# Performance work log

Measured on AMD Instinct MI355X. Metric: run time of the kernel, lower is better.

## Reference

```python
import jax, jax.numpy as jnp
import numpy as np
from jax import lax

FILTERS = 8      # Conv1D filters per column
K = 5            # kernel_size
ACTION_DIM = 2
COLS = [16, 128, 1024]  # columns entering each of the 3 blocks (grow x FILTERS)


def setup_inputs() -> dict:
    key = jax.random.key(0)
    ks = jax.random.split(key, 8)
    B, L, C = 64, 128, 16
    state = jax.random.normal(ks[0], (B, L, C), jnp.float32)
    inp = {"state": state}
    # One grouped-conv kernel per block: WIO layout [K, in_per_group=1, cols*FILTERS].
    # Channel c*FILTERS+f of the output is column c's filter f (matches Keras concat order).
    for i, c in enumerate(COLS):
        inp[f"k{i+1}"] = jax.random.normal(ks[1 + i], (K, 1, c * FILTERS), jnp.float32) * 0.1
        inp[f"b{i+1}"] = jnp.zeros((c * FILTERS,), jnp.float32)
    L_final = L - len(COLS) * (K - 1)          # 116
    feat = L_final * COLS[-1] * FILTERS        # 950272
    inp["W"] = jax.random.normal(ks[4], (feat, ACTION_DIM), jnp.float32) * 1e-3
    inp["bd"] = jnp.zeros((ACTION_DIM,), jnp.float32)
    return inp


def _block(x, kern, bias):
    # x: [B, cols, L]  ->  [B, cols*FILTERS, L-K+1]
    cols = x.shape[1]
    xin = jnp.transpose(x, (0, 2, 1))  # [B, L, cols] (NWC)
    y = lax.conv_general_dilated(
        xin, kern, window_strides=(1,), padding='VALID',
        dimension_numbers=('NWC', 'WIO', 'NWC'), feature_group_count=cols)
    y = jax.nn.relu(y + bias)          # [B, L', cols*FILTERS]
    return jnp.transpose(y, (0, 2, 1))


def reference(state, k1, b1, k2, b2, k3, b3, W, bd):
    # Actor.call: transpose [B,L,C] -> [B,C,L], run blocks, transpose back, flatten, dense+tanh
    x = jnp.transpose(state, (0, 2, 1))  # [B, cols=16, L=128]
    for kern, bias in ((k1, b1), (k2, b2), (k3, b3)):
        x = _block(x, kern, bias)
    x = jnp.transpose(x, (0, 2, 1)).reshape(state.shape[0], -1)  # [B, L'*channels]
    return jnp.tanh(x @ W + bd)  # [B, ACTION_DIM]
```

## Files before the change

kernel.cpp:

```cpp
#include <hip/hip_runtime.h>
#include <math.h>

#define NB    64
#define L0    128
#define C0    16
#define KW    5
#define NF    8
#define L1    124
#define L2    120
#define L3    116
#define CH1   128
#define CH2   1024
#define CH3   8192
#define NCHUNK 8
#define NS     4
#define SLICE  29
#define TROWS  (SLICE + 4)
#define Y1R    (SLICE + 8)
#define STR    (SLICE + 12)

__global__ __launch_bounds__(128, 4) void actor_fused_kernel(
    const float* __restrict__ state,
    const float* __restrict__ k1,
    const float* __restrict__ b1,
    const float* __restrict__ k2,
    const float* __restrict__ b2,
    const float* __restrict__ k3,
    const float* __restrict__ b3,
    const float* __restrict__ W,
    float* __restrict__ partials)
{
    const int chunk = blockIdx.x;
    const int b     = blockIdx.y;
    const int slice = blockIdx.z;
    const int t0    = slice * SLICE;
    const int tid   = threadIdx.x;
    const int c3    = chunk * 128 + tid;

    __shared__ float s_state[STR][2];
    __shared__ float s_y1[Y1R][16];
    __shared__ float tile[TROWS][128];

    for (int idx = tid; idx < STR * 2; idx += 128) {
        int r = idx >> 1, c = idx & 1;
        s_state[r][c] = state[(size_t)b * L0 * C0 + (t0 + r) * C0 + chunk * 2 + c];
    }
    __syncthreads();

    for (int idx = tid; idx < Y1R * 16; idx += 128) {
        int r = idx >> 4, jloc = idx & 15;
        int j = chunk * 16 + jloc;
        int cloc = jloc >> 3;
        float acc = b1[j];
#pragma unroll
        for (int k = 0; k < KW; ++k)
            acc = fmaf(s_state[r + k][cloc], k1[k * CH1 + j], acc);
        s_y1[r][jloc] = fmaxf(acc, 0.f);
    }
    __syncthreads();

    {
        int m = chunk * 128 + tid;
        int jloc = tid >> 3;
        float kk[KW], bb = b2[m];
#pragma unroll
        for (int k = 0; k < KW; ++k) kk[k] = k2[k * CH2 + m];
        for (int r = 0; r < TROWS; ++r) {
            float acc = bb;
#pragma unroll
            for (int k = 0; k < KW; ++k)
                acc = fmaf(s_y1[r + k][jloc], kk[k], acc);
            tile[r][tid] = fmaxf(acc, 0.f);
        }
    }

    float kw[KW][NF], bv[NF];
#pragma unroll
    for (int k = 0; k < KW; ++k)
#pragma unroll
        for (int f = 0; f < NF; ++f)
            kw[k][f] = k3[k * CH3 + c3 * NF + f];
#pragma unroll
    for (int f = 0; f < NF; ++f)
        bv[f] = b3[c3 * NF + f];

    float a0x = 0.f, a0y = 0.f, a1x = 0.f, a1y = 0.f;
    float a2x = 0.f, a2y = 0.f, a3x = 0.f, a3y = 0.f;

    const float4* __restrict__ W4 = (const float4*)W;

    float w0 = tile[0][tid];
    float w1 = tile[1][tid];
    float w2 = tile[2][tid];
    float w3 = tile[3][tid];

    for (int t = 0; t < SLICE; ++t) {
        float w4 = tile[t + 4][tid];

        float v[NF];
#pragma unroll
        for (int f = 0; f < NF; ++f) {
            float a = bv[f];
            a = fmaf(w0, kw[0][f], a);
            a = fmaf(w1, kw[1][f], a);
            a = fmaf(w2, kw[2][f], a);
            a = fmaf(w3, kw[3][f], a);
            a = fmaf(w4, kw[4][f], a);
            v[f] = fmaxf(a, 0.f);
        }

        size_t base4 = (size_t)(t0 + t) * 4096 + (size_t)c3 * 4;
        float4 q0 = W4[base4 + 0];
        float4 q1 = W4[base4 + 1];
        float4 q2 = W4[base4 + 2];
        float4 q3 = W4[base4 + 3];

        a0x = fmaf(v[0], q0.x, a0x); a0y = fmaf(v[0], q0.y, a0y);
        a0x = fmaf(v[1], q0.z, a0x); a0y = fmaf(v[1], q0.w, a0y);
        a1x = fmaf(v[2], q1.x, a1x); a1y = fmaf(v[2], q1.y, a1y);
        a1x = fmaf(v[3], q1.z, a1x); a1y = fmaf(v[3], q1.w, a1y);
        a2x = fmaf(v[4], q2.x, a2x); a2y = fmaf(v[4], q2.y, a2y);
        a2x = fmaf(v[5], q2.z, a2x); a2y = fmaf(v[5], q2.w, a2y);
        a3x = fmaf(v[6], q3.x, a3x); a3y = fmaf(v[6], q3.y, a3y);
        a3x = fmaf(v[7], q3.z, a3x); a3y = fmaf(v[7], q3.w, a3y);

        w0 = w1; w1 = w2; w2 = w3; w3 = w4;
    }

    float acc0 = (a0x + a1x) + (a2x + a3x);
    float acc1 = (a0y + a1y) + (a2y + a3y);

#pragma unroll
    for (int d = 32; d >= 1; d >>= 1) {
        acc0 += __shfl_down(acc0, d, 64);
        acc1 += __shfl_down(acc1, d, 64);
    }
    __shared__ float red[2][2];
    int wave = tid >> 6, lane = tid & 63;
    if (lane == 0) { red[wave][0] = acc0; red[wave][1] = acc1; }
    __syncthreads();
    if (tid == 0) {
        size_t o = (((size_t)b * NCHUNK + chunk) * NS + slice) * 2;
        partials[o + 0] = red[0][0] + red[1][0];
        partials[o + 1] = red[0][1] + red[1][1];
    }
}

__global__ __launch_bounds__(128) void finish_kernel(
    const float* __restrict__ partials,
    const float* __restrict__ bd,
    float* __restrict__ out)
{
    int i = threadIdx.x;
    int b = i >> 1, a = i & 1;
    float s = bd[a];
#pragma unroll
    for (int p = 0; p < NCHUNK * NS; ++p)
        s += partials[((size_t)b * NCHUNK * NS + p) * 2 + a];
    out[b * 2 + a] = tanhf(s);
}

extern "C" void kernel_launch(void* const* d_in, const int* in_sizes, int n_in,
                              void* d_out, int out_size, void* d_ws, size_t ws_size,
                              hipStream_t stream) {
    const float* state = (const float*)d_in[0];
    const float* k1    = (const float*)d_in[1];
    const float* b1    = (const float*)d_in[2];
    const float* k2    = (const float*)d_in[3];
    const float* b2    = (const float*)d_in[4];
    const float* k3    = (const float*)d_in[5];
    const float* b3    = (const float*)d_in[6];
    const float* W     = (const float*)d_in[7];
    const float* bd    = (const float*)d_in[8];
    float* out = (float*)d_out;

    float* partials = (float*)d_ws;

    dim3 grid(NCHUNK, NB, NS);
    actor_fused_kernel<<<grid, 128, 0, stream>>>(
        state, k1, b1, k2, b2, k3, b3, W, partials);

    finish_kernel<<<1, 128, 0, stream>>>(partials, bd, out);
}
```

Before: 105.3 us.

## Split each layer-3 column's filters across two threads with 256-thread blocks

Doubles the block size to 256 threads. Each pair of threads now handles one layer-3 column, each taking half of the 8 filters and half of the W float4 loads. The layer-2 tile computation is split between the two 128-thread halves, and a barrier is added because threads now read tile columns written by other threads. This halves per-thread registers and serial work to raise occupancy and memory-level parallelism. The cost is redundant tile reads and an extra barrier.

After: 98.38 us. -6.5%, faster.

```diff
diff --git a/kernel.cpp b/kernel.cpp
--- a/kernel.cpp
+++ b/kernel.cpp
@@ -18,8 +18,9 @@
 #define TROWS  (SLICE + 4)
 #define Y1R    (SLICE + 8)
 #define STR    (SLICE + 12)
+#define NFH    4
 
-__global__ __launch_bounds__(128, 4) void actor_fused_kernel(
+__global__ __launch_bounds__(256, 8) void actor_fused_kernel(
     const float* __restrict__ state,
     const float* __restrict__ k1,
     const float* __restrict__ b1,
@@ -35,19 +36,21 @@
     const int slice = blockIdx.z;
     const int t0    = slice * SLICE;
     const int tid   = threadIdx.x;
-    const int c3    = chunk * 128 + tid;
+    const int c3loc = tid >> 1;
+    const int fh    = tid & 1;
+    const int c3    = chunk * 128 + c3loc;
 
     __shared__ float s_state[STR][2];
     __shared__ float s_y1[Y1R][16];
     __shared__ float tile[TROWS][128];
 
-    for (int idx = tid; idx < STR * 2; idx += 128) {
-        int r = idx >> 1, c = idx & 1;
+    if (tid < STR * 2) {
+        int r = tid >> 1, c = tid & 1;
         s_state[r][c] = state[(size_t)b * L0 * C0 + (t0 + r) * C0 + chunk * 2 + c];
     }
     __syncthreads();
 
-    for (int idx = tid; idx < Y1R * 16; idx += 128) {
+    for (int idx = tid; idx < Y1R * 16; idx += 256) {
         int r = idx >> 4, jloc = idx & 15;
         int j = chunk * 16 + jloc;
         int cloc = jloc >> 3;
@@ -60,46 +63,50 @@
     __syncthreads();
 
     {
-        int m = chunk * 128 + tid;
-        int jloc = tid >> 3;
+        int c = tid & 127, h = tid >> 7;
+        int m = chunk * 128 + c;
+        int jloc = c >> 3;
         float kk[KW], bb = b2[m];
 #pragma unroll
         for (int k = 0; k < KW; ++k) kk[k] = k2[k * CH2 + m];
-        for (int r = 0; r < TROWS; ++r) {
+        int r0 = h ? 17 : 0, r1 = h ? TROWS : 17;
+        for (int r = r0; r < r1; ++r) {
             float acc = bb;
 #pragma unroll
             for (int k = 0; k < KW; ++k)
                 acc = fmaf(s_y1[r + k][jloc], kk[k], acc);
-            tile[r][tid] = fmaxf(acc, 0.f);
+            tile[r][c] = fmaxf(acc, 0.f);
         }
     }
 
-    float kw[KW][NF], bv[NF];
+    float kw[KW][NFH], bv[NFH];
 #pragma unroll
     for (int k = 0; k < KW; ++k)
 #pragma unroll
-        for (int f = 0; f < NF; ++f)
-            kw[k][f] = k3[k * CH3 + c3 * NF + f];
+        for (int f = 0; f < NFH; ++f)
+            kw[k][f] = k3[k * CH3 + c3 * NF + fh * NFH + f];
 #pragma unroll
-    for (int f = 0; f < NF; ++f)
-        bv[f] = b3[c3 * NF + f];
+    for (int f = 0; f < NFH; ++f)
+        bv[f] = b3[c3 * NF + fh * NFH + f];
+
+    __syncthreads();
 
     float a0x = 0.f, a0y = 0.f, a1x = 0.f, a1y = 0.f;
-    float a2x = 0.f, a2y = 0.f, a3x = 0.f, a3y = 0.f;
 
-    const float4* __restrict__ W4 = (const float4*)W;
+    const float4* __restrict__ wp =
+        (const float4*)W + (size_t)t0 * 4096 + (size_t)c3 * 4 + fh * 2;
 
-    float w0 = tile[0][tid];
-    float w1 = tile[1][tid];
-    float w2 = tile[2][tid];
-    float w3 = tile[3][tid];
+    float w0 = tile[0][c3loc];
+    float w1 = tile[1][c3loc];
+    float w2 = tile[2][c3loc];
+    float w3 = tile[3][c3loc];
 
     for (int t = 0; t < SLICE; ++t) {
-        float w4 = tile[t + 4][tid];
+        float w4 = tile[t + 4][c3loc];
 
-        float v[NF];
+        float v[NFH];
 #pragma unroll
-        for (int f = 0; f < NF; ++f) {
+        for (int f = 0; f < NFH; ++f) {
             float a = bv[f];
             a = fmaf(w0, kw[0][f], a);
             a = fmaf(w1, kw[1][f], a);
@@ -109,40 +116,34 @@
             v[f] = fmaxf(a, 0.f);
         }
 
-        size_t base4 = (size_t)(t0 + t) * 4096 + (size_t)c3 * 4;
-        float4 q0 = W4[base4 + 0];
-        float4 q1 = W4[base4 + 1];
-        float4 q2 = W4[base4 + 2];
-        float4 q3 = W4[base4 + 3];
+        float4 q0 = wp[0];
+        float4 q1 = wp[1];
+        wp += 4096;
 
         a0x = fmaf(v[0], q0.x, a0x); a0y = fmaf(v[0], q0.y, a0y);
         a0x = fmaf(v[1], q0.z, a0x); a0y = fmaf(v[1], q0.w, a0y);
         a1x = fmaf(v[2], q1.x, a1x); a1y = fmaf(v[2], q1.y, a1y);
         a1x = fmaf(v[3], q1.z, a1x); a1y = fmaf(v[3], q1.w, a1y);
-        a2x = fmaf(v[4], q2.x, a2x); a2y = fmaf(v[4], q2.y, a2y);
-        a2x = fmaf(v[5], q2.z, a2x); a2y = fmaf(v[5], q2.w, a2y);
-        a3x = fmaf(v[6], q3.x, a3x); a3y = fmaf(v[6], q3.y, a3y);
-        a3x = fmaf(v[7], q3.z, a3x); a3y = fmaf(v[7], q3.w, a3y);
 
         w0 = w1; w1 = w2; w2 = w3; w3 = w4;
     }
 
-    float acc0 = (a0x + a1x) + (a2x + a3x);
-    float acc1 = (a0y + a1y) + (a2y + a3y);
+    float acc0 = a0x + a1x;
+    float acc1 = a0y + a1y;
 
 #pragma unroll
     for (int d = 32; d >= 1; d >>= 1) {
         acc0 += __shfl_down(acc0, d, 64);
         acc1 += __shfl_down(acc1, d, 64);
     }
-    __shared__ float red[2][2];
+    __shared__ float red[4][2];
     int wave = tid >> 6, lane = tid & 63;
     if (lane == 0) { red[wave][0] = acc0; red[wave][1] = acc1; }
     __syncthreads();
     if (tid == 0) {
         size_t o = (((size_t)b * NCHUNK + chunk) * NS + slice) * 2;
-        partials[o + 0] = red[0][0] + red[1][0];
-        partials[o + 1] = red[0][1] + red[1][1];
+        partials[o + 0] = (red[0][0] + red[1][0]) + (red[2][0] + red[3][0]);
+        partials[o + 1] = (red[0][1] + red[1][1]) + (red[2][1] + red[3][1]);
     }
 }
 
@@ -177,7 +178,7 @@
     float* partials = (float*)d_ws;
 
     dim3 grid(NCHUNK, NB, NS);
-    actor_fused_kernel<<<grid, 128, 0, stream>>>(
+    actor_fused_kernel<<<grid, 256, 0, stream>>>(
         state, k1, b1, k2, b2, k3, b3, W, partials);
 
     finish_kernel<<<1, 128, 0, stream>>>(partials, bd, out);
```
